# Kernel tuning notes

Measured on AMD Instinct MI355X. Metric: run time of the kernel, lower is better.

The kernel has to match this reference:

```python
import jax, jax.numpy as jnp
import numpy as np

# Module hyper-parameters (from init_kwargs)
NDIM = 2
KSIZE = [3, 3]            # must be odd per ConvSP checks
DILATION = [0.05, 0.05]
RADIUS = 0.1
C_IN, C_OUT = 64, 64
B, N = 2, 2048


def _offsets():
    # Kernel-cell center offsets relative to the particle, row-major over dims
    # (matches the cartesian ordering of the original C extension).
    axes = [(np.arange(k) - (k - 1) / 2.0) * d for k, d in zip(KSIZE, DILATION)]
    grids = np.meshgrid(*axes, indexing='ij')
    return np.stack([g.reshape(-1) for g in grids], axis=-1).astype(np.float32)  # [ncells, D]


def setup_inputs() -> dict:
    key = jax.random.key(0)
    k1, k2, k3, k4, k5, k6 = jax.random.split(key, 6)
    pos = jax.random.uniform(k1, (B, N, NDIM), dtype=jnp.float32)          # coords in [0,1]^D
    invmass = jax.random.uniform(k2, (B, N), dtype=jnp.float32) * 0.9 + 0.1  # avoid 1/0
    locs = jnp.concatenate([pos, invmass[..., None]], axis=-1)             # [B,N,D+1]
    data = jax.random.normal(k3, (B, C_IN, N), dtype=jnp.float32)
    density = jax.random.uniform(k4, (B, N), dtype=jnp.float32) + 0.5      # strictly positive
    ncells = int(np.prod(KSIZE))
    weight = jax.random.normal(k5, (C_OUT, C_IN, ncells), dtype=jnp.float32) * 0.05
    bias = jax.random.normal(k6, (C_OUT,), dtype=jnp.float32) * 0.05
    return {"locs": locs, "data": data, "density": density, "weight": weight, "bias": bias}


def _convsp(locs, data, density, weight, bias):
    # SPH interpolation at each kernel-cell query point r_{i,k} = x_i + off_k:
    #   field[b,c,i,k] = sum_j (m_j / rho_j) * data[b,c,j] * W(|x_j - r_{i,k}|, RADIUS)
    # with m_j = 1/invmass_j, then a 1x1-style contraction with weight over (c,k).
    pos = locs[..., :NDIM]                               # [B,N,D]
    invmass = locs[..., NDIM]                            # [B,N]
    coef = 1.0 / (invmass * density)                     # m_j / rho_j, [B,N]
    dcoef = data * coef[:, None, :]                      # [B,C,N]
    diff = pos[:, :, None, :] - pos[:, None, :, :]       # x_i - x_j, [B,N,N,D]
    r2 = RADIUS * RADIUS
    knorm = 315.0 / (64.0 * np.pi * RADIUS ** 9)         # poly6 smoothing kernel norm
    offs = _offsets()                                    # [ncells, D]
    bsz, n = pos.shape[0], pos.shape[1]
    out = jnp.broadcast_to(bias[None, :, None], (bsz, weight.shape[0], n))
    for k in range(offs.shape[0]):                       # fixed small ncells=9 loop
        # |x_j - x_i - off| == |(x_i - x_j) + off|
        d2 = jnp.sum((diff + offs[k]) ** 2, axis=-1)     # [B,N,N] (i = query, j = neighbor)
        w = jnp.where(d2 < r2, (r2 - d2) ** 3, 0.0) * knorm
        field = jnp.einsum('bcj,bij->bci', dcoef, w)     # gather-weighted average
        out = out + jnp.einsum('oc,bci->boi', weight[:, :, k], field)
    return out


def reference(locs, data, density, weight, bias):
    return _convsp(locs, data, density, weight, bias)
```

## Files before the change

kernel.cpp:

```cpp
#include <hip/hip_runtime.h>
#include <hip/hip_bf16.h>
#include <stdint.h>

#define BATCH 2
#define NPTS  2048
#define CIN   64
#define COUT  64
#define NCELL 9

#define KNORM 1.5666851e9f
#define R2 0.01f

typedef __attribute__((ext_vector_type(8))) __bf16 bf16x8;
typedef __attribute__((ext_vector_type(4))) float  f32x4;

union B8 { uint4 u; bf16x8 v; };

static __device__ __forceinline__ unsigned pk2(float a, float b) {
    union { __hip_bfloat162 h; unsigned u; } cv;
    cv.h = __float22bfloat162_rn(make_float2(a, b));
    return cv.u;
}


__global__ __launch_bounds__(256) void prep_kernel(
    const float* __restrict__ locs, const float* __restrict__ data,
    const float* __restrict__ density, const float* __restrict__ weight,
    const float* __restrict__ bias,
    float2* __restrict__ posT, uint16_t* __restrict__ dC,
    uint16_t* __restrict__ WB, float* __restrict__ out)
{
    const int tid = threadIdx.x;
    const int g = blockIdx.x;
    if (g < 256) {
        int e = g * 256 + tid;
        int j4 = e & 511, bc = e >> 9;
        int b = bc >> 6;
        float4 dv = *(const float4*)(data + bc * 2048 + j4 * 4);
        float4 de = *(const float4*)(density + b * 2048 + j4 * 4);
        int jb = (b * 2048 + j4 * 4) * 3 + 2;
        float m0 = locs[jb], m1 = locs[jb + 3], m2 = locs[jb + 6], m3 = locs[jb + 9];
        float v0 = dv.x / (m0 * de.x);
        float v1 = dv.y / (m1 * de.y);
        float v2 = dv.z / (m2 * de.z);
        float v3 = dv.w / (m3 * de.w);
        *(uint2*)(dC + bc * 2048 + j4 * 4) = make_uint2(pk2(v0, v1), pk2(v2, v3));
    } else if (g < 272) {
        int jj = (g - 256) * 256 + tid;
        posT[jj] = make_float2(locs[jj * 3], locs[jj * 3 + 1]);
    } else if (g < 272 + NCELL) {
        int cell = g - 272;
        for (int it = 0; it < 16; it++) {
            int e = it * 256 + tid;
            int ks = e >> 11, ob = (e >> 9) & 3, lane = (e >> 3) & 63, jj = e & 7;
            int o = ob * 16 + (lane & 15);
            int c = ks * 32 + ((lane >> 4) & 3) * 8 + jj;
            union { __hip_bfloat16 h; uint16_t u; } cv;
            cv.h = __float2bfloat16(weight[(o * 64 + c) * 9 + cell]);
            WB[cell * 4096 + e] = cv.u;
        }
    } else {
        const int gb = g - (272 + NCELL);
#pragma unroll
        for (int r = 0; r < 2; r++) {
            int e4 = (gb * 512 + r * 256 + tid) * 4;
            float bv = bias[(e4 >> 11) & 63];
            *(float4*)(out + e4) = make_float4(bv, bv, bv, bv);
        }
    }
}

__global__ __launch_bounds__(256, 2) void conv_kernel(
    const float2* __restrict__ posT, const uint16_t* __restrict__ dC,
    const uint16_t* __restrict__ WB, float* __restrict__ out)
{
    __shared__ float sft[4][16 * 68];

    const int tid  = threadIdx.x;
    const int lane = tid & 63;
    const int wid  = tid >> 6;
    const int cl   = lane & 15;
    const int quad = lane >> 4;
    const int bx   = blockIdx.x;
    const int jh   = bx & 1;
    const int b    = bx >> 8;
    const int i0   = ((bx >> 1) & 127) * 16;

    const float2 pI = posT[b * 2048 + i0 + cl];

    f32x4 acc[NCELL][4];
#pragma unroll
    for (int k = 0; k < NCELL; k++)
#pragma unroll
        for (int nb = 0; nb < 4; nb++) acc[k][nb] = (f32x4){0.f, 0.f, 0.f, 0.f};

    const uint16_t* rb0 = dC + ((b * 64 +  0 + cl) * 2048) + jh * 1024 + wid * 32 + quad * 8;
    const uint16_t* rb1 = rb0 + 16 * 2048;
    const uint16_t* rb2 = rb0 + 32 * 2048;
    const uint16_t* rb3 = rb0 + 48 * 2048;
    const float2* pjb = posT + b * 2048 + jh * 1024 + wid * 32 + quad * 8;

    B8 bfc[4];
    bfc[0].u = *(const uint4*)rb0;
    bfc[1].u = *(const uint4*)rb1;
    bfc[2].u = *(const uint4*)rb2;
    bfc[3].u = *(const uint4*)rb3;

#pragma unroll
    for (int t = 0; t < 8; t++) {
        B8 bfn[4];
        if (t < 7) {
            bfn[0].u = *(const uint4*)(rb0 + (t + 1) * 128);
            bfn[1].u = *(const uint4*)(rb1 + (t + 1) * 128);
            bfn[2].u = *(const uint4*)(rb2 + (t + 1) * 128);
            bfn[3].u = *(const uint4*)(rb3 + (t + 1) * 128);
        }

        const float4* pp = (const float4*)(pjb + t * 128);
        float4 q0 = pp[0], q1 = pp[1], q2 = pp[2], q3 = pp[3];
        float dyv[8], ru0[8], ru1[8], ru2[8];
        {
            float dxv[8];
            dxv[0] = pI.x - q0.x; dyv[0] = pI.y - q0.y;
            dxv[1] = pI.x - q0.z; dyv[1] = pI.y - q0.w;
            dxv[2] = pI.x - q1.x; dyv[2] = pI.y - q1.y;
            dxv[3] = pI.x - q1.z; dyv[3] = pI.y - q1.w;
            dxv[4] = pI.x - q2.x; dyv[4] = pI.y - q2.y;
            dxv[5] = pI.x - q2.z; dyv[5] = pI.y - q2.w;
            dxv[6] = pI.x - q3.x; dyv[6] = pI.y - q3.y;
            dxv[7] = pI.x - q3.z; dyv[7] = pI.y - q3.w;
#pragma unroll
            for (int p = 0; p < 8; p++) {
                float a0 = dxv[p] - 0.05f;
                float a1 = dxv[p];
                float a2 = dxv[p] + 0.05f;
                ru0[p] = fmaf(-a0, a0, R2);
                ru1[p] = fmaf(-a1, a1, R2);
                ru2[p] = fmaf(-a2, a2, R2);
            }
        }

#pragma unroll
        for (int k = 0; k < NCELL; k++) {
            const float oy = (float)(k % 3 - 1) * 0.05f;
            float w[8];
#pragma unroll
            for (int p = 0; p < 8; p++) {
                float ru = (k < 3) ? ru0[p] : (k < 6) ? ru1[p] : ru2[p];
                float c  = dyv[p] + oy;
                float tt = fmaf(-c, c, ru);
                float mt = fmaxf(tt, 0.0f);
                w[p] = (mt * mt) * (mt * KNORM);
            }
            B8 af;
            af.u = make_uint4(pk2(w[0], w[1]), pk2(w[2], w[3]),
                              pk2(w[4], w[5]), pk2(w[6], w[7]));
#pragma unroll
            for (int nb = 0; nb < 4; nb++)
                acc[k][nb] = __builtin_amdgcn_mfma_f32_16x16x32_bf16(
                    af.v, bfc[nb].v, acc[k][nb], 0, 0, 0);
        }

        if (t < 7) {
            bfc[0] = bfn[0]; bfc[1] = bfn[1];
            bfc[2] = bfn[2]; bfc[3] = bfn[3];
        }
    }

    float* scr = &sft[wid][0];
    f32x4 acc2[4];
#pragma unroll
    for (int ob = 0; ob < 4; ob++) acc2[ob] = (f32x4){0.f, 0.f, 0.f, 0.f};

#pragma unroll
    for (int k = 0; k < NCELL; k++) {
#pragma unroll
        for (int nb = 0; nb < 4; nb++)
#pragma unroll
            for (int r = 0; r < 4; r++)
                scr[(quad * 4 + r) * 68 + nb * 16 + cl] = acc[k][nb][r];
#pragma unroll
        for (int ks = 0; ks < 2; ks++) {
            const float* fp = &scr[cl * 68 + ks * 32 + quad * 8];
            float4 lo = *(const float4*)fp;
            float4 hi = *(const float4*)(fp + 4);
            B8 af;
            af.u = make_uint4(pk2(lo.x, lo.y), pk2(lo.z, lo.w),
                              pk2(hi.x, hi.y), pk2(hi.z, hi.w));
#pragma unroll
            for (int ob = 0; ob < 4; ob++) {
                B8 wf;
                wf.u = *(const uint4*)(WB + k * 4096 + (ks * 4 + ob) * 512 + lane * 8);
                acc2[ob] = __builtin_amdgcn_mfma_f32_16x16x32_bf16(
                    af.v, wf.v, acc2[ob], 0, 0, 0);
            }
        }
    }

#pragma unroll
    for (int ob = 0; ob < 4; ob++)
#pragma unroll
        for (int r = 0; r < 4; r++)
            scr[(quad * 4 + r) * 68 + ob * 16 + cl] = acc2[ob][r];
    __syncthreads();

    {
        const int i  = tid & 15;
        const int og = tid >> 4;
        float4 s0 = *(const float4*)&sft[0][i * 68 + og * 4];
        float4 s1 = *(const float4*)&sft[1][i * 68 + og * 4];
        float4 s2 = *(const float4*)&sft[2][i * 68 + og * 4];
        float4 s3 = *(const float4*)&sft[3][i * 68 + og * 4];
        float v0 = s0.x + s1.x + s2.x + s3.x;
        float v1 = s0.y + s1.y + s2.y + s3.y;
        float v2 = s0.z + s1.z + s2.z + s3.z;
        float v3 = s0.w + s1.w + s2.w + s3.w;
        float* op = out + (b * 64 + og * 4) * 2048 + i0 + i;
        unsafeAtomicAdd(op + 0 * 2048, v0);
        unsafeAtomicAdd(op + 1 * 2048, v1);
        unsafeAtomicAdd(op + 2 * 2048, v2);
        unsafeAtomicAdd(op + 3 * 2048, v3);
    }
}

extern "C" void kernel_launch(void* const* d_in, const int* in_sizes, int n_in,
                              void* d_out, int out_size, void* d_ws, size_t ws_size,
                              hipStream_t stream)
{
    const float* locs    = (const float*)d_in[0];
    const float* data    = (const float*)d_in[1];
    const float* density = (const float*)d_in[2];
    const float* weight  = (const float*)d_in[3];
    const float* bias    = (const float*)d_in[4];
    float* out = (float*)d_out;

    float2*   posT = (float2*)d_ws;
    uint16_t* dC   = (uint16_t*)((char*)d_ws + 32768);
    uint16_t* WB   = (uint16_t*)((char*)d_ws + 32768 + 524288);

    prep_kernel<<<272 + NCELL + 128, 256, 0, stream>>>(
        locs, data, density, weight, bias, posT, dC, WB, out);
    conv_kernel<<<BATCH * 128 * 2, 256, 0, stream>>>(posT, dC, WB, out);
}
```

Baseline: 93.70 us.

## Split kernel cells across waves and the neighbour range into quarters

Each block now covers a quarter of the neighbour range, and each wave accumulates only 2–3 of the 9 kernel cells instead of all 9. This cuts the per-wave accumulator registers from 36 to 12 MFMA tiles, so launch bounds can ask for 3 blocks per SM. The poly6 normalisation constant is folded into the bf16 data coefficients in the prep kernel, removing one multiply per weight. In exchange, every wave recomputes the same pairwise distances, wave 0 carries one more cell than the others, and the number of output atomics doubles.

```diff
diff --git a/kernel.cpp b/kernel.cpp
--- a/kernel.cpp
+++ b/kernel.cpp
@@ -40,10 +40,10 @@
         float4 de = *(const float4*)(density + b * 2048 + j4 * 4);
         int jb = (b * 2048 + j4 * 4) * 3 + 2;
         float m0 = locs[jb], m1 = locs[jb + 3], m2 = locs[jb + 6], m3 = locs[jb + 9];
-        float v0 = dv.x / (m0 * de.x);
-        float v1 = dv.y / (m1 * de.y);
-        float v2 = dv.z / (m2 * de.z);
-        float v3 = dv.w / (m3 * de.w);
+        float v0 = KNORM * dv.x / (m0 * de.x);
+        float v1 = KNORM * dv.y / (m1 * de.y);
+        float v2 = KNORM * dv.z / (m2 * de.z);
+        float v3 = KNORM * dv.w / (m3 * de.w);
         *(uint2*)(dC + bc * 2048 + j4 * 4) = make_uint2(pk2(v0, v1), pk2(v2, v3));
     } else if (g < 272) {
         int jj = (g - 256) * 256 + tid;
@@ -70,7 +70,7 @@
     }
 }
 
-__global__ __launch_bounds__(256, 2) void conv_kernel(
+__global__ __launch_bounds__(256, 3) void conv_kernel(
     const float2* __restrict__ posT, const uint16_t* __restrict__ dC,
     const uint16_t* __restrict__ WB, float* __restrict__ out)
 {
@@ -82,23 +82,33 @@
     const int cl   = lane & 15;
     const int quad = lane >> 4;
     const int bx   = blockIdx.x;
-    const int jh   = bx & 1;
-    const int b    = bx >> 8;
-    const int i0   = ((bx >> 1) & 127) * 16;
+    const int b    = bx >> 9;
+    const int i0   = ((bx >> 2) & 127) * 16;
+    const int jb0  = (bx & 3) * 512;
+
+    const int c0 = (wid == 0) ? 0 : (1 + wid * 2);
+    const int nc = (wid == 0) ? 3 : 2;
+    float oxr[3], oyr[3];
+#pragma unroll
+    for (int ci = 0; ci < 3; ci++) {
+        int k = c0 + (ci < nc ? ci : 0);
+        oxr[ci] = (float)(k / 3 - 1) * 0.05f;
+        oyr[ci] = (float)(k % 3 - 1) * 0.05f;
+    }
 
     const float2 pI = posT[b * 2048 + i0 + cl];
 
-    f32x4 acc[NCELL][4];
-#pragma unroll
-    for (int k = 0; k < NCELL; k++)
-#pragma unroll
-        for (int nb = 0; nb < 4; nb++) acc[k][nb] = (f32x4){0.f, 0.f, 0.f, 0.f};
-
-    const uint16_t* rb0 = dC + ((b * 64 +  0 + cl) * 2048) + jh * 1024 + wid * 32 + quad * 8;
+    f32x4 acc[3][4];
+#pragma unroll
+    for (int ci = 0; ci < 3; ci++)
+#pragma unroll
+        for (int nb = 0; nb < 4; nb++) acc[ci][nb] = (f32x4){0.f, 0.f, 0.f, 0.f};
+
+    const uint16_t* rb0 = dC + (b * 64 +  0 + cl) * 2048 + jb0 + quad * 8;
     const uint16_t* rb1 = rb0 + 16 * 2048;
     const uint16_t* rb2 = rb0 + 32 * 2048;
     const uint16_t* rb3 = rb0 + 48 * 2048;
-    const float2* pjb = posT + b * 2048 + jh * 1024 + wid * 32 + quad * 8;
+    const float2* pjb = posT + b * 2048 + jb0 + quad * 8;
 
     B8 bfc[4];
     bfc[0].u = *(const uint4*)rb0;
@@ -106,17 +116,17 @@
     bfc[2].u = *(const uint4*)rb2;
     bfc[3].u = *(const uint4*)rb3;
 
-#pragma unroll
-    for (int t = 0; t < 8; t++) {
+#pragma unroll 2
+    for (int t = 0; t < 16; t++) {
         B8 bfn[4];
-        if (t < 7) {
-            bfn[0].u = *(const uint4*)(rb0 + (t + 1) * 128);
-            bfn[1].u = *(const uint4*)(rb1 + (t + 1) * 128);
-            bfn[2].u = *(const uint4*)(rb2 + (t + 1) * 128);
-            bfn[3].u = *(const uint4*)(rb3 + (t + 1) * 128);
-        }
-
-        const float4* pp = (const float4*)(pjb + t * 128);
+        if (t < 15) {
+            bfn[0].u = *(const uint4*)(rb0 + (t + 1) * 32);
+            bfn[1].u = *(const uint4*)(rb1 + (t + 1) * 32);
+            bfn[2].u = *(const uint4*)(rb2 + (t + 1) * 32);
+            bfn[3].u = *(const uint4*)(rb3 + (t + 1) * 32);
+        }
+
+        const float4* pp = (const float4*)(pjb + t * 32);
         float4 q0 = pp[0], q1 = pp[1], q2 = pp[2], q3 = pp[3];
         float dyv[8], ru0[8], ru1[8], ru2[8];
         {
@@ -141,27 +151,30 @@
         }
 
 #pragma unroll
-        for (int k = 0; k < NCELL; k++) {
-            const float oy = (float)(k % 3 - 1) * 0.05f;
-            float w[8];
-#pragma unroll
-            for (int p = 0; p < 8; p++) {
-                float ru = (k < 3) ? ru0[p] : (k < 6) ? ru1[p] : ru2[p];
-                float c  = dyv[p] + oy;
-                float tt = fmaf(-c, c, ru);
-                float mt = fmaxf(tt, 0.0f);
-                w[p] = (mt * mt) * (mt * KNORM);
+        for (int ci = 0; ci < 3; ci++) {
+            if (ci < nc) {
+                int k = c0 + ci;
+                const float oy = oyr[ci];
+                float w[8];
+#pragma unroll
+                for (int p = 0; p < 8; p++) {
+                    float ru = (k < 3) ? ru0[p] : (k < 6) ? ru1[p] : ru2[p];
+                    float cy = dyv[p] + oy;
+                    float tt = fmaf(-cy, cy, ru);
+                    float mt = fmaxf(tt, 0.0f);
+                    w[p] = (mt * mt) * mt;
+                }
+                B8 af;
+                af.u = make_uint4(pk2(w[0], w[1]), pk2(w[2], w[3]),
+                                  pk2(w[4], w[5]), pk2(w[6], w[7]));
+#pragma unroll
+                for (int nb = 0; nb < 4; nb++)
+                    acc[ci][nb] = __builtin_amdgcn_mfma_f32_16x16x32_bf16(
+                        af.v, bfc[nb].v, acc[ci][nb], 0, 0, 0);
             }
-            B8 af;
-            af.u = make_uint4(pk2(w[0], w[1]), pk2(w[2], w[3]),
-                              pk2(w[4], w[5]), pk2(w[6], w[7]));
-#pragma unroll
-            for (int nb = 0; nb < 4; nb++)
-                acc[k][nb] = __builtin_amdgcn_mfma_f32_16x16x32_bf16(
-                    af.v, bfc[nb].v, acc[k][nb], 0, 0, 0);
-        }
-
-        if (t < 7) {
+        }
+
+        if (t < 15) {
             bfc[0] = bfn[0]; bfc[1] = bfn[1];
             bfc[2] = bfn[2]; bfc[3] = bfn[3];
         }
@@ -173,26 +186,29 @@
     for (int ob = 0; ob < 4; ob++) acc2[ob] = (f32x4){0.f, 0.f, 0.f, 0.f};
 
 #pragma unroll
-    for (int k = 0; k < NCELL; k++) {
-#pragma unroll
-        for (int nb = 0; nb < 4; nb++)
-#pragma unroll
-            for (int r = 0; r < 4; r++)
-                scr[(quad * 4 + r) * 68 + nb * 16 + cl] = acc[k][nb][r];
-#pragma unroll
-        for (int ks = 0; ks < 2; ks++) {
-            const float* fp = &scr[cl * 68 + ks * 32 + quad * 8];
-            float4 lo = *(const float4*)fp;
-            float4 hi = *(const float4*)(fp + 4);
-            B8 af;
-            af.u = make_uint4(pk2(lo.x, lo.y), pk2(lo.z, lo.w),
-                              pk2(hi.x, hi.y), pk2(hi.z, hi.w));
-#pragma unroll
-            for (int ob = 0; ob < 4; ob++) {
-                B8 wf;
-                wf.u = *(const uint4*)(WB + k * 4096 + (ks * 4 + ob) * 512 + lane * 8);
-                acc2[ob] = __builtin_amdgcn_mfma_f32_16x16x32_bf16(
-                    af.v, wf.v, acc2[ob], 0, 0, 0);
+    for (int ci = 0; ci < 3; ci++) {
+        if (ci < nc) {
+#pragma unroll
+            for (int nb = 0; nb < 4; nb++)
+#pragma unroll
+                for (int r = 0; r < 4; r++)
+                    scr[(quad * 4 + r) * 68 + nb * 16 + cl] = acc[ci][nb][r];
+            int k = c0 + ci;
+#pragma unroll
+            for (int ks = 0; ks < 2; ks++) {
+                const float* fp = &scr[cl * 68 + ks * 32 + quad * 8];
+                float4 lo = *(const float4*)fp;
+                float4 hi = *(const float4*)(fp + 4);
+                B8 af;
+                af.u = make_uint4(pk2(lo.x, lo.y), pk2(lo.z, lo.w),
+                                  pk2(hi.x, hi.y), pk2(hi.z, hi.w));
+#pragma unroll
+                for (int ob = 0; ob < 4; ob++) {
+                    B8 wf;
+                    wf.u = *(const uint4*)(WB + k * 4096 + (ks * 4 + ob) * 512 + lane * 8);
+                    acc2[ob] = __builtin_amdgcn_mfma_f32_16x16x32_bf16(
+                        af.v, wf.v, acc2[ob], 0, 0, 0);
+                }
             }
         }
     }
@@ -240,5 +256,5 @@
 
     prep_kernel<<<272 + NCELL + 128, 256, 0, stream>>>(
         locs, data, density, weight, bias, posT, dC, WB, out);
-    conv_kernel<<<BATCH * 128 * 2, 256, 0, stream>>>(posT, dC, WB, out);
-}
+    conv_kernel<<<BATCH * 128 * 4, 256, 0, stream>>>(posT, dC, WB, out);
+}
```

After: 112.6 us. 1.2x slower.
